# Performance work log

Measured on AMD Instinct MI355X. Metric: run time of the kernel, lower is better.

Reference implementation:

```python
import jax, jax.numpy as jnp
import numpy as np

NUM_CAPSULE = 16
DIM_CAPSULE = 32
ROUTINGS = 3
EPS = 1e-7  # K.epsilon()


def _squash(x):
    # NOTE: this repo's squash is x / sqrt(sum(x^2) + eps), i.e. pure normalization
    s = jnp.sum(jnp.square(x), axis=-1, keepdims=True)
    return x / jnp.sqrt(s + EPS)


def setup_inputs() -> dict:
    key = jax.random.key(0)
    k1, k2 = jax.random.split(key)
    B, S, D_in = 256, 512, 256
    u_vecs = jax.random.normal(k1, (B, S, D_in), dtype=jnp.float32)
    # shared conv1d kernel, kernel width 1: (1, input_dim, num_capsule*dim_capsule)
    W = jax.random.normal(k2, (1, D_in, NUM_CAPSULE * DIM_CAPSULE), dtype=jnp.float32) * 0.05
    return {"u_vecs": u_vecs, "W": W}


def reference(u_vecs, W):
    B, S, _ = u_vecs.shape
    # K.conv1d with kernel size 1 == pointwise projection
    u_hat = jnp.einsum('bsi,io->bso', u_vecs, W[0])
    # (B, S, nc*dc) -> (B, nc, S, dc)
    u_hat = u_hat.reshape(B, S, NUM_CAPSULE, DIM_CAPSULE).transpose(0, 2, 1, 3)
    b = jnp.zeros((B, NUM_CAPSULE, S), dtype=u_hat.dtype)
    outputs = None
    for i in range(ROUTINGS):
        # softmax over the num_capsule axis (permute->softmax(last)->permute back)
        c = jax.nn.softmax(b, axis=1)  # (B, nc, S)
        outputs = _squash(jnp.einsum('bni,bnid->bnd', c, u_hat))  # (B, nc, dc)
        if i < ROUTINGS - 1:
            b = jnp.einsum('bnd,bnid->bni', outputs, u_hat)
    return outputs
```

## Files before the change

kernel.cpp:

```cpp
#include <hip/hip_runtime.h>


#define SDIM 512
#define DIN  256
#define NCAP 16
#define DCAP 32
#define OC   512

typedef __attribute__((ext_vector_type(8))) __bf16 bf16x8;
typedef __attribute__((ext_vector_type(4))) float f32x4;
typedef __attribute__((ext_vector_type(4))) unsigned short u16x4;

static_assert(sizeof(bf16x8) == 16, "bf16x8 must be 16B");

__device__ __forceinline__ unsigned short f2bf(float f) {
  unsigned u = __float_as_uint(f);
  u += 0x7FFFu + ((u >> 16) & 1u);
  return (unsigned short)(u >> 16);
}

__global__ __launch_bounds__(1024) void caps_fused(
    const float* __restrict__ Uall, const float* __restrict__ Wg,
    float* __restrict__ outp)
{
  __shared__ __align__(16) unsigned short sU16[64 * 256];
  __shared__ __align__(16) unsigned short sWt16[16 * 256];
  __shared__ __align__(16) unsigned short sCT16[16 * 64];
  __shared__ __align__(16) float sV[16 * 256];
  __shared__ __align__(16) float sOut[512];

  float* sSS = (float*)sCT16;

  const int tid = threadIdx.x;
  const int w = tid >> 6;
  const int l = tid & 63;
  const int b = blockIdx.x;
  const float* U = Uall + (size_t)b * (SDIM * DIN);
  const float4* g4 = (const float4*)U;

  {
    float4 a = make_float4(0.f, 0.f, 0.f, 0.f);
    const int base = (w * 32) * 64 + l;
    #pragma unroll 8
    for (int r = 0; r < 32; ++r) {
      float4 v = g4[base + r * 64];
      a.x += v.x; a.y += v.y; a.z += v.z; a.w += v.w;
    }
    *(float4*)&sV[w * 256 + 4 * l] = a;
  }
  __syncthreads();
  if (tid < 256) {
    float s = 0.f;
    #pragma unroll
    for (int q = 0; q < 16; ++q) s += sV[q * 256 + tid];
    sSS[tid] = s * (1.0f / 16.0f);
  }
  __syncthreads();

  auto outCompute = [&](int mode) {
    if (tid < 512) {
      const int c = tid;
      const int n = c >> 5;
      float p0 = 0.f, p1 = 0.f, p2 = 0.f, p3 = 0.f;
      #pragma unroll 4
      for (int i = 0; i < 256; i += 4) {
        float x0 = mode ? sV[n * 256 + i + 0] : sSS[i + 0];
        float x1 = mode ? sV[n * 256 + i + 1] : sSS[i + 1];
        float x2 = mode ? sV[n * 256 + i + 2] : sSS[i + 2];
        float x3 = mode ? sV[n * 256 + i + 3] : sSS[i + 3];
        p0 = fmaf(Wg[(i + 0) * OC + c], x0, p0);
        p1 = fmaf(Wg[(i + 1) * OC + c], x1, p1);
        p2 = fmaf(Wg[(i + 2) * OC + c], x2, p2);
        p3 = fmaf(Wg[(i + 3) * OC + c], x3, p3);
      }
      float p = (p0 + p1) + (p2 + p3);
      float sq = p * p;
      #pragma unroll
      for (int off = 1; off < 32; off <<= 1) sq += __shfl_xor(sq, off);
      sOut[c] = p * rsqrtf(sq + 1e-7f);
    }
    __syncthreads();
  };

  auto wtCompute = [&]() {
    const int f4 = tid & 127;
    const int rr = tid >> 7;
    const float4 ov = *(const float4*)&sOut[4 * f4];
    #pragma unroll 4
    for (int it = 0; it < 32; ++it) {
      const int i = it * 8 + rr;
      const float4 wv = *(const float4*)&Wg[i * OC + 4 * f4];
      float p = wv.x * ov.x + wv.y * ov.y + wv.z * ov.z + wv.w * ov.w;
      p += __shfl_xor(p, 1);
      p += __shfl_xor(p, 2);
      p += __shfl_xor(p, 4);
      if ((f4 & 7) == 0) {
        const int n = f4 >> 3;
        sWt16[(n * 256 + i) ^ ((n & 7) << 3)] = f2bf(p);
      }
    }
    __syncthreads();
  };

  auto stage = [&](const float4* pre) {
    #pragma unroll
    for (int k = 0; k < 4; ++k) {
      const int s = w + 16 * k;
      u16x4 h;
      h[0] = f2bf(pre[k].x); h[1] = f2bf(pre[k].y);
      h[2] = f2bf(pre[k].z); h[3] = f2bf(pre[k].w);
      *(u16x4*)&sU16[(s * 256 + 4 * l) ^ ((s & 7) << 3)] = h;
    }
  };

  auto pass = [&]() {
    f32x4 vacc = {0.f, 0.f, 0.f, 0.f};
    const int nr = l & 15;
    const int grp = l >> 4;
    {
      float4 pre[4];
      #pragma unroll
      for (int k = 0; k < 4; ++k) pre[k] = g4[(w + 16 * k) * 64 + l];
      stage(pre);
    }
    __syncthreads();
    for (int chunk = 0; chunk < 8; ++chunk) {
      float4 nxt[4];
      if (chunk < 7) {
        #pragma unroll
        for (int k = 0; k < 4; ++k)
          nxt[k] = g4[((chunk + 1) * 64 + w + 16 * k) * 64 + l];
      }
      if (w < 4) {
        f32x4 y = {0.f, 0.f, 0.f, 0.f};
        const int arow = 16 * w + nr;
        #pragma unroll
        for (int ks = 0; ks < 8; ++ks) {
          bf16x8 a = *(const bf16x8*)&sU16[(arow * 256 + ks * 32 + grp * 8) ^ ((arow & 7) << 3)];
          bf16x8 bw = *(const bf16x8*)&sWt16[(nr * 256 + ks * 32 + grp * 8) ^ ((nr & 7) << 3)];
          y = __builtin_amdgcn_mfma_f32_16x16x32_bf16(a, bw, y, 0, 0, 0);
        }
        float y0 = y[0], y1 = y[1], y2 = y[2], y3 = y[3];
        float m0 = y0, m1 = y1, m2 = y2, m3 = y3;
        #pragma unroll
        for (int off = 1; off < 16; off <<= 1) {
          m0 = fmaxf(m0, __shfl_xor(m0, off));
          m1 = fmaxf(m1, __shfl_xor(m1, off));
          m2 = fmaxf(m2, __shfl_xor(m2, off));
          m3 = fmaxf(m3, __shfl_xor(m3, off));
        }
        float e0 = __expf(y0 - m0), e1 = __expf(y1 - m1);
        float e2 = __expf(y2 - m2), e3 = __expf(y3 - m3);
        float s0 = e0, s1 = e1, s2 = e2, s3 = e3;
        #pragma unroll
        for (int off = 1; off < 16; off <<= 1) {
          s0 += __shfl_xor(s0, off);
          s1 += __shfl_xor(s1, off);
          s2 += __shfl_xor(s2, off);
          s3 += __shfl_xor(s3, off);
        }
        u16x4 cw;
        cw[0] = f2bf(e0 / s0); cw[1] = f2bf(e1 / s1);
        cw[2] = f2bf(e2 / s2); cw[3] = f2bf(e3 / s3);
        *(u16x4*)&sCT16[(nr * 64 + 16 * w + 4 * grp) ^ ((nr & 7) << 3)] = cw;
      }
      __syncthreads();
      {
        const int icol = 16 * w + nr;
        #pragma unroll
        for (int ks = 0; ks < 2; ++ks) {
          bf16x8 a = *(const bf16x8*)&sCT16[(nr * 64 + ks * 32 + grp * 8) ^ ((nr & 7) << 3)];
          bf16x8 bb;
          const int s0b = ks * 32 + grp * 8;
          #pragma unroll
          for (int j = 0; j < 8; ++j) {
            unsigned short v = sU16[((s0b + j) * 256 + icol) ^ (j << 3)];
            bb[j] = __builtin_bit_cast(__bf16, v);
          }
          vacc = __builtin_amdgcn_mfma_f32_16x16x32_bf16(a, bb, vacc, 0, 0, 0);
        }
      }
      __syncthreads();
      if (chunk < 7) stage(nxt);
      __syncthreads();
    }
    #pragma unroll
    for (int r = 0; r < 4; ++r) sV[(grp * 4 + r) * 256 + 16 * w + nr] = vacc[r];
    __syncthreads();
  };

  outCompute(0);
  wtCompute();
  pass();
  outCompute(1);
  wtCompute();
  pass();
  outCompute(1);

  if (tid < 512) outp[(size_t)b * 512 + tid] = sOut[tid];
}

extern "C" void kernel_launch(void* const* d_in, const int* in_sizes, int n_in,
                              void* d_out, int out_size, void* d_ws, size_t ws_size,
                              hipStream_t stream) {
  const float* u = (const float*)d_in[0];
  const float* Wg = (const float*)d_in[1];
  float* out = (float*)d_out;
  dim3 grid(256), block(1024);
  hipLaunchKernelGGL(caps_fused, grid, block, 0, stream, u, Wg, out);
}
```

Baseline: 262.1 us.

## Warp-specialize U staging with double-buffered 128-row LDS chunks

Waves are split into roles: waves 8-15 load and convert the next 128-row chunk of U into a second LDS buffer while waves 0-7 run the logit MFMAs and softmax on the current chunk. Chunks grow from 64 to 128 rows and syncs per chunk drop from three to two, which cuts barrier count and overlaps global loads with compute. The first chunk is prefetched into registers before the out/Wt setup, and the second pass's first chunk is staged during the tail of the first pass. The change needs about 160KB of dynamic LDS and drops the max-subtraction from the softmax, which risks overflow if logits grow large.

```diff
diff --git a/kernel.cpp b/kernel.cpp
--- a/kernel.cpp
+++ b/kernel.cpp
@@ -1,11 +1,11 @@
 #include <hip/hip_runtime.h>
 
 
-#define SDIM 512
-#define DIN  256
-#define NCAP 16
-#define DCAP 32
-#define OC   512
+#define SROWS 512
+#define DIN   256
+#define OC    512
+#define CH    128
+#define NCH   4
 
 typedef __attribute__((ext_vector_type(8))) __bf16 bf16x8;
 typedef __attribute__((ext_vector_type(4))) float f32x4;
@@ -19,27 +19,27 @@
   return (unsigned short)(u >> 16);
 }
 
-__global__ __launch_bounds__(1024) void caps_fused(
+
+__global__ __launch_bounds__(1024) void caps_main(
     const float* __restrict__ Uall, const float* __restrict__ Wg,
     float* __restrict__ outp)
 {
-  __shared__ __align__(16) unsigned short sU16[64 * 256];
-  __shared__ __align__(16) unsigned short sWt16[16 * 256];
-  __shared__ __align__(16) unsigned short sCT16[16 * 64];
-  __shared__ __align__(16) float sV[16 * 256];
-  __shared__ __align__(16) float sOut[512];
-
-  float* sSS = (float*)sCT16;
+  extern __shared__ char smem[];
+  unsigned short* sU  = (unsigned short*)smem;
+  unsigned short* sWt = (unsigned short*)(smem + 131072);
+  unsigned short* sCT = (unsigned short*)(smem + 139264);
+  float* sV   = (float*)(smem + 143360);
+  float* sOut = (float*)(smem + 159744);
+  float* sSS  = (float*)(smem + 139264);
 
   const int tid = threadIdx.x;
-  const int w = tid >> 6;
-  const int l = tid & 63;
+  const int w = tid >> 6, l = tid & 63;
+  const int nr = l & 15, g = l >> 4;
   const int b = blockIdx.x;
-  const float* U = Uall + (size_t)b * (SDIM * DIN);
-  const float4* g4 = (const float4*)U;
+  const float4* g4 = (const float4*)(Uall + (size_t)b * (SROWS * DIN));
 
   {
-    float4 a = make_float4(0.f, 0.f, 0.f, 0.f);
+    float4 a = {0.f, 0.f, 0.f, 0.f};
     const int base = (w * 32) * 64 + l;
     #pragma unroll 8
     for (int r = 0; r < 32; ++r) {
@@ -57,10 +57,13 @@
   }
   __syncthreads();
 
+  float4 pre[8];
+  #pragma unroll
+  for (int k = 0; k < 8; ++k) pre[k] = g4[(w * 8 + k) * 64 + l];
+
   auto outCompute = [&](int mode) {
     if (tid < 512) {
-      const int c = tid;
-      const int n = c >> 5;
+      const int c = tid, n = c >> 5;
       float p0 = 0.f, p1 = 0.f, p2 = 0.f, p3 = 0.f;
       #pragma unroll 4
       for (int i = 0; i < 256; i += 4) {
@@ -96,105 +99,101 @@
       p += __shfl_xor(p, 4);
       if ((f4 & 7) == 0) {
         const int n = f4 >> 3;
-        sWt16[(n * 256 + i) ^ ((n & 7) << 3)] = f2bf(p);
+        sWt[(n * 256 + i) ^ ((n & 7) << 3)] = f2bf(p);
       }
     }
     __syncthreads();
   };
 
-  auto stage = [&](const float4* pre) {
-    #pragma unroll
-    for (int k = 0; k < 4; ++k) {
-      const int s = w + 16 * k;
+  auto writePre = [&]() {
+    #pragma unroll
+    for (int k = 0; k < 8; ++k) {
+      const int rl = w * 8 + k;
       u16x4 h;
       h[0] = f2bf(pre[k].x); h[1] = f2bf(pre[k].y);
       h[2] = f2bf(pre[k].z); h[3] = f2bf(pre[k].w);
-      *(u16x4*)&sU16[(s * 256 + 4 * l) ^ ((s & 7) << 3)] = h;
-    }
-  };
-
-  auto pass = [&]() {
+      *(u16x4*)&sU[(rl * 256 + 4 * l) ^ ((rl & 7) << 3)] = h;
+    }
+  };
+
+  auto stage8 = [&](int p, int rbase) {
+    const int wi = w - 8;
+    #pragma unroll
+    for (int h = 0; h < 2; ++h) {
+      float4 v[8];
+      #pragma unroll
+      for (int k = 0; k < 8; ++k) v[k] = g4[(rbase + wi * 16 + h * 8 + k) * 64 + l];
+      #pragma unroll
+      for (int k = 0; k < 8; ++k) {
+        const int rl = wi * 16 + h * 8 + k;
+        u16x4 hh;
+        hh[0] = f2bf(v[k].x); hh[1] = f2bf(v[k].y);
+        hh[2] = f2bf(v[k].z); hh[3] = f2bf(v[k].w);
+        *(u16x4*)&sU[p * 32768 + ((rl * 256 + 4 * l) ^ ((rl & 7) << 3))] = hh;
+      }
+    }
+  };
+
+  auto pass = [&](bool stageNext) {
     f32x4 vacc = {0.f, 0.f, 0.f, 0.f};
-    const int nr = l & 15;
-    const int grp = l >> 4;
-    {
-      float4 pre[4];
-      #pragma unroll
-      for (int k = 0; k < 4; ++k) pre[k] = g4[(w + 16 * k) * 64 + l];
-      stage(pre);
-    }
-    __syncthreads();
-    for (int chunk = 0; chunk < 8; ++chunk) {
-      float4 nxt[4];
-      if (chunk < 7) {
-        #pragma unroll
-        for (int k = 0; k < 4; ++k)
-          nxt[k] = g4[((chunk + 1) * 64 + w + 16 * k) * 64 + l];
-      }
-      if (w < 4) {
+    for (int c = 0; c < NCH; ++c) {
+      const int p = c & 1;
+      if (w >= 8) {
+        if (c < NCH - 1)      stage8(p ^ 1, (c + 1) * CH);
+        else if (stageNext)   stage8(p ^ 1, 0);
+      } else {
         f32x4 y = {0.f, 0.f, 0.f, 0.f};
         const int arow = 16 * w + nr;
+        const int asw = (nr & 7) << 3;
         #pragma unroll
         for (int ks = 0; ks < 8; ++ks) {
-          bf16x8 a = *(const bf16x8*)&sU16[(arow * 256 + ks * 32 + grp * 8) ^ ((arow & 7) << 3)];
-          bf16x8 bw = *(const bf16x8*)&sWt16[(nr * 256 + ks * 32 + grp * 8) ^ ((nr & 7) << 3)];
+          bf16x8 a  = *(const bf16x8*)&sU[p * 32768 + ((arow * 256 + ks * 32 + g * 8) ^ asw)];
+          bf16x8 bw = *(const bf16x8*)&sWt[(nr * 256 + ks * 32 + g * 8) ^ asw];
           y = __builtin_amdgcn_mfma_f32_16x16x32_bf16(a, bw, y, 0, 0, 0);
         }
-        float y0 = y[0], y1 = y[1], y2 = y[2], y3 = y[3];
-        float m0 = y0, m1 = y1, m2 = y2, m3 = y3;
-        #pragma unroll
-        for (int off = 1; off < 16; off <<= 1) {
-          m0 = fmaxf(m0, __shfl_xor(m0, off));
-          m1 = fmaxf(m1, __shfl_xor(m1, off));
-          m2 = fmaxf(m2, __shfl_xor(m2, off));
-          m3 = fmaxf(m3, __shfl_xor(m3, off));
-        }
-        float e0 = __expf(y0 - m0), e1 = __expf(y1 - m1);
-        float e2 = __expf(y2 - m2), e3 = __expf(y3 - m3);
+        float e0 = __expf(y[0]), e1 = __expf(y[1]), e2 = __expf(y[2]), e3 = __expf(y[3]);
         float s0 = e0, s1 = e1, s2 = e2, s3 = e3;
         #pragma unroll
         for (int off = 1; off < 16; off <<= 1) {
-          s0 += __shfl_xor(s0, off);
-          s1 += __shfl_xor(s1, off);
-          s2 += __shfl_xor(s2, off);
-          s3 += __shfl_xor(s3, off);
+          s0 += __shfl_xor(s0, off); s1 += __shfl_xor(s1, off);
+          s2 += __shfl_xor(s2, off); s3 += __shfl_xor(s3, off);
         }
         u16x4 cw;
         cw[0] = f2bf(e0 / s0); cw[1] = f2bf(e1 / s1);
         cw[2] = f2bf(e2 / s2); cw[3] = f2bf(e3 / s3);
-        *(u16x4*)&sCT16[(nr * 64 + 16 * w + 4 * grp) ^ ((nr & 7) << 3)] = cw;
+        *(u16x4*)&sCT[(nr * 128 + 16 * w + 4 * g) ^ asw] = cw;
       }
       __syncthreads();
       {
         const int icol = 16 * w + nr;
         #pragma unroll
-        for (int ks = 0; ks < 2; ++ks) {
-          bf16x8 a = *(const bf16x8*)&sCT16[(nr * 64 + ks * 32 + grp * 8) ^ ((nr & 7) << 3)];
+        for (int ks = 0; ks < 4; ++ks) {
+          bf16x8 a = *(const bf16x8*)&sCT[(nr * 128 + ks * 32 + g * 8) ^ ((nr & 7) << 3)];
           bf16x8 bb;
-          const int s0b = ks * 32 + grp * 8;
           #pragma unroll
           for (int j = 0; j < 8; ++j) {
-            unsigned short v = sU16[((s0b + j) * 256 + icol) ^ (j << 3)];
-            bb[j] = __builtin_bit_cast(__bf16, v);
+            const int s = ks * 32 + g * 8 + j;
+            bb[j] = __builtin_bit_cast(__bf16,
+                     sU[p * 32768 + ((s * 256 + icol) ^ ((s & 7) << 3))]);
           }
           vacc = __builtin_amdgcn_mfma_f32_16x16x32_bf16(a, bb, vacc, 0, 0, 0);
         }
       }
       __syncthreads();
-      if (chunk < 7) stage(nxt);
-      __syncthreads();
-    }
-    #pragma unroll
-    for (int r = 0; r < 4; ++r) sV[(grp * 4 + r) * 256 + 16 * w + nr] = vacc[r];
+    }
+    #pragma unroll
+    for (int r = 0; r < 4; ++r) sV[(4 * g + r) * 256 + 16 * w + nr] = vacc[r];
     __syncthreads();
   };
 
   outCompute(0);
   wtCompute();
-  pass();
+  writePre();
+  __syncthreads();
+  pass(true);
   outCompute(1);
   wtCompute();
-  pass();
+  pass(false);
   outCompute(1);
 
   if (tid < 512) outp[(size_t)b * 512 + tid] = sOut[tid];
@@ -203,9 +202,11 @@
 extern "C" void kernel_launch(void* const* d_in, const int* in_sizes, int n_in,
                               void* d_out, int out_size, void* d_ws, size_t ws_size,
                               hipStream_t stream) {
-  const float* u = (const float*)d_in[0];
+  const float* u  = (const float*)d_in[0];
   const float* Wg = (const float*)d_in[1];
   float* out = (float*)d_out;
-  dim3 grid(256), block(1024);
-  hipLaunchKernelGGL(caps_fused, grid, block, 0, stream, u, Wg, out);
+  (void)d_ws; (void)ws_size;
+  hipFuncSetAttribute(reinterpret_cast<const void*>(caps_main),
+                      hipFuncAttributeMaxDynamicSharedMemorySize, 161792);
+  caps_main<<<dim3(256), dim3(1024), 161792, stream>>>(u, Wg, out);
 }
```

Measured after the change: 279.3 us. +6.6%, slower.

## Split fused capsule routing into multi-kernel pipeline with row-split parallelism

Applied to the files above, without the earlier changes.

Replaces the single per-batch fused kernel (256 blocks of 1024 threads) with a sequence of kernels: a column-sum kernel, a routing kernel that computes squashed outputs and W·out projections, and a pass kernel that splits each batch's 512 sequence rows across 4 blocks and writes partial sums to workspace. This is meant to raise the number of concurrently active blocks and cut per-block serialization, at the cost of extra launches and global round-trips through workspace. It also drops the max-subtraction in the softmax, relying on logits being bounded because the outputs are normalized. The old fused kernel is kept as a fallback when the workspace is too small.

```diff
diff --git a/kernel.cpp b/kernel.cpp
--- a/kernel.cpp
+++ b/kernel.cpp
@@ -1,22 +1,205 @@
 #include <hip/hip_runtime.h>
 
 
-#define SDIM 512
-#define DIN  256
-#define NCAP 16
-#define DCAP 32
-#define OC   512
+#define DIN   256
+#define OC    512
+#define SROWS 512
 
 typedef __attribute__((ext_vector_type(8))) __bf16 bf16x8;
 typedef __attribute__((ext_vector_type(4))) float f32x4;
 typedef __attribute__((ext_vector_type(4))) unsigned short u16x4;
-
-static_assert(sizeof(bf16x8) == 16, "bf16x8 must be 16B");
 
 __device__ __forceinline__ unsigned short f2bf(float f) {
   unsigned u = __float_as_uint(f);
   u += 0x7FFFu + ((u >> 16) & 1u);
   return (unsigned short)(u >> 16);
+}
+
+#define SWZ(r) ((((r) ^ ((r) >> 3)) & 7) << 3)
+
+__global__ __launch_bounds__(256) void k_colsum(
+    const float* __restrict__ Uall, float* __restrict__ cpart)
+{
+  __shared__ float sA[4][256];
+  const int t = blockIdx.x, b = blockIdx.y;
+  const int tid = threadIdx.x;
+  const int c4 = tid & 63, rq = tid >> 6;
+  const float4* g4 = (const float4*)(Uall + (size_t)b * (SROWS * DIN));
+  const int R0 = t * 128;
+  float4 a = {0.f, 0.f, 0.f, 0.f};
+  #pragma unroll 8
+  for (int k = 0; k < 32; ++k) {
+    float4 v = g4[(R0 + rq + 4 * k) * 64 + c4];
+    a.x += v.x; a.y += v.y; a.z += v.z; a.w += v.w;
+  }
+  *(float4*)&sA[rq][4 * c4] = a;
+  __syncthreads();
+  if (tid < 64) {
+    float4 s = {0.f, 0.f, 0.f, 0.f};
+    #pragma unroll
+    for (int q = 0; q < 4; ++q) {
+      float4 v = *(float4*)&sA[q][4 * tid];
+      s.x += v.x; s.y += v.y; s.z += v.z; s.w += v.w;
+    }
+    *(float4*)&cpart[(size_t)(b * 4 + t) * 256 + 4 * tid] = s;
+  }
+}
+
+__global__ __launch_bounds__(512) void k_route(
+    const float* __restrict__ W, const float* __restrict__ src,
+    unsigned short* __restrict__ wt, float* __restrict__ outF,
+    int mode, int final_)
+{
+  __shared__ float sV[16 * 256];
+  __shared__ float sP[2][512];
+  __shared__ float sOut[512];
+  const int b = blockIdx.x;
+  const int tid = threadIdx.x;
+
+  if (mode == 0) {
+    if (tid < 256) {
+      float v = 0.f;
+      #pragma unroll
+      for (int t = 0; t < 4; ++t) v += src[(size_t)(b * 4 + t) * 256 + tid];
+      #pragma unroll
+      for (int n = 0; n < 16; ++n) sV[n * 256 + tid] = v;
+    }
+  } else {
+    #pragma unroll
+    for (int qq = 0; qq < 2; ++qq) {
+      const int q = 2 * tid + qq;
+      f32x4 s = {0.f, 0.f, 0.f, 0.f};
+      #pragma unroll
+      for (int t = 0; t < 4; ++t)
+        s += *(const f32x4*)&src[(size_t)(b * 4 + t) * 4096 + 4 * q];
+      *(f32x4*)&sV[4 * q] = s;
+    }
+  }
+  __syncthreads();
+
+  {
+    const int pair = tid & 255, half = tid >> 8;
+    const int c0 = pair * 2, n = c0 >> 5;
+    float p0 = 0.f, p1 = 0.f;
+    const int i0 = half * 128;
+    #pragma unroll 8
+    for (int i = i0; i < i0 + 128; ++i) {
+      const float2 wv = *(const float2*)&W[(size_t)i * OC + c0];
+      const float x = sV[n * 256 + i];
+      p0 = fmaf(wv.x, x, p0);
+      p1 = fmaf(wv.y, x, p1);
+    }
+    sP[half][c0] = p0; sP[half][c0 + 1] = p1;
+  }
+  __syncthreads();
+
+  {
+    const float p = sP[0][tid] + sP[1][tid];
+    float sq = p * p;
+    #pragma unroll
+    for (int off = 1; off < 32; off <<= 1) sq += __shfl_xor(sq, off);
+    const float o = p * rsqrtf(sq + 1e-7f);
+    if (final_) { outF[(size_t)b * 512 + tid] = o; return; }
+    sOut[tid] = o;
+  }
+  __syncthreads();
+
+  {
+    const int f4i = tid & 127, rr = tid >> 7;
+    const int n = f4i >> 3;
+    const float4 ov = *(const float4*)&sOut[4 * f4i];
+    #pragma unroll 4
+    for (int it = 0; it < 64; ++it) {
+      const int i = it * 4 + rr;
+      const float4 wv = *(const float4*)&W[(size_t)i * OC + 4 * f4i];
+      float p = wv.x * ov.x + wv.y * ov.y + wv.z * ov.z + wv.w * ov.w;
+      p += __shfl_xor(p, 1);
+      p += __shfl_xor(p, 2);
+      p += __shfl_xor(p, 4);
+      if ((tid & 7) == 0)
+        wt[(size_t)b * 4096 + n * 256 + i] = f2bf(p);
+    }
+  }
+}
+
+__global__ __launch_bounds__(512, 4) void k_pass(
+    const float* __restrict__ Uall, const unsigned short* __restrict__ wt,
+    float* __restrict__ vpart)
+{
+  extern __shared__ char smem[];
+  unsigned short* sU  = (unsigned short*)smem;
+  unsigned short* sWt = (unsigned short*)(smem + 65536);
+  unsigned short* sCT = (unsigned short*)(smem + 73728);
+
+  const int t = blockIdx.x, b = blockIdx.y;
+  const int tid = threadIdx.x;
+  const int w = tid >> 6, l = tid & 63;
+  const int nr = l & 15, g = l >> 4;
+  const float4* g4 = (const float4*)(Uall + (size_t)b * (SROWS * DIN));
+  const int R0 = t * 128;
+
+  {
+    const int n = tid >> 5, i0 = (tid & 31) * 8;
+    const uint4 wv = *(const uint4*)&wt[(size_t)b * 4096 + n * 256 + i0];
+    *(uint4*)&sWt[(n * 256 + i0) ^ SWZ(n)] = wv;
+  }
+  #pragma unroll 4
+  for (int k = 0; k < 16; ++k) {
+    const int row = w * 16 + k;
+    const float4 v = g4[(R0 + row) * 64 + l];
+    u16x4 h;
+    h[0] = f2bf(v.x); h[1] = f2bf(v.y); h[2] = f2bf(v.z); h[3] = f2bf(v.w);
+    *(u16x4*)&sU[(row * 256 + 4 * l) ^ SWZ(row)] = h;
+  }
+  __syncthreads();
+
+  {
+    f32x4 y = {0.f, 0.f, 0.f, 0.f};
+    const int arow = 16 * w + nr;
+    #pragma unroll
+    for (int ks = 0; ks < 8; ++ks) {
+      bf16x8 a  = *(const bf16x8*)&sU[(arow * 256 + ks * 32 + g * 8) ^ SWZ(arow)];
+      bf16x8 bw = *(const bf16x8*)&sWt[(nr * 256 + ks * 32 + g * 8) ^ SWZ(nr)];
+      y = __builtin_amdgcn_mfma_f32_16x16x32_bf16(a, bw, y, 0, 0, 0);
+    }
+    float e0 = __expf(y[0]), e1 = __expf(y[1]), e2 = __expf(y[2]), e3 = __expf(y[3]);
+    float s0 = e0, s1 = e1, s2 = e2, s3 = e3;
+    #pragma unroll
+    for (int off = 1; off < 16; off <<= 1) {
+      s0 += __shfl_xor(s0, off); s1 += __shfl_xor(s1, off);
+      s2 += __shfl_xor(s2, off); s3 += __shfl_xor(s3, off);
+    }
+    u16x4 cw;
+    cw[0] = f2bf(e0 / s0); cw[1] = f2bf(e1 / s1);
+    cw[2] = f2bf(e2 / s2); cw[3] = f2bf(e3 / s3);
+    *(u16x4*)&sCT[(nr * 128 + 16 * w + 4 * g) ^ SWZ(nr)] = cw;
+  }
+  __syncthreads();
+
+  {
+    const int icol0 = 32 * w + nr, icol1 = icol0 + 16;
+    f32x4 v0 = {0.f, 0.f, 0.f, 0.f}, v1 = {0.f, 0.f, 0.f, 0.f};
+    #pragma unroll
+    for (int ks = 0; ks < 4; ++ks) {
+      bf16x8 a = *(const bf16x8*)&sCT[(nr * 128 + ks * 32 + g * 8) ^ SWZ(nr)];
+      bf16x8 b0, b1;
+      #pragma unroll
+      for (int j = 0; j < 8; ++j) {
+        const int s = ks * 32 + g * 8 + j;
+        b0[j] = __builtin_bit_cast(__bf16, sU[(s * 256 + icol0) ^ SWZ(s)]);
+        b1[j] = __builtin_bit_cast(__bf16, sU[(s * 256 + icol1) ^ SWZ(s)]);
+      }
+      v0 = __builtin_amdgcn_mfma_f32_16x16x32_bf16(a, b0, v0, 0, 0, 0);
+      v1 = __builtin_amdgcn_mfma_f32_16x16x32_bf16(a, b1, v1, 0, 0, 0);
+    }
+    float* vp = vpart + (size_t)(b * 4 + t) * 4096;
+    #pragma unroll
+    for (int r = 0; r < 4; ++r) {
+      const int n = 4 * g + r;
+      vp[n * 256 + icol0] = v0[r];
+      vp[n * 256 + icol1] = v1[r];
+    }
+  }
 }
 
 __global__ __launch_bounds__(1024) void caps_fused(
@@ -28,14 +211,12 @@
   __shared__ __align__(16) unsigned short sCT16[16 * 64];
   __shared__ __align__(16) float sV[16 * 256];
   __shared__ __align__(16) float sOut[512];
-
   float* sSS = (float*)sCT16;
 
   const int tid = threadIdx.x;
-  const int w = tid >> 6;
-  const int l = tid & 63;
+  const int w = tid >> 6, l = tid & 63;
   const int b = blockIdx.x;
-  const float* U = Uall + (size_t)b * (SDIM * DIN);
+  const float* U = Uall + (size_t)b * (SROWS * DIN);
   const float4* g4 = (const float4*)U;
 
   {
@@ -59,8 +240,7 @@
 
   auto outCompute = [&](int mode) {
     if (tid < 512) {
-      const int c = tid;
-      const int n = c >> 5;
+      const int c = tid, n = c >> 5;
       float p0 = 0.f, p1 = 0.f, p2 = 0.f, p3 = 0.f;
       #pragma unroll 4
       for (int i = 0; i < 256; i += 4) {
@@ -140,24 +320,12 @@
           bf16x8 bw = *(const bf16x8*)&sWt16[(nr * 256 + ks * 32 + grp * 8) ^ ((nr & 7) << 3)];
           y = __builtin_amdgcn_mfma_f32_16x16x32_bf16(a, bw, y, 0, 0, 0);
         }
-        float y0 = y[0], y1 = y[1], y2 = y[2], y3 = y[3];
-        float m0 = y0, m1 = y1, m2 = y2, m3 = y3;
-        #pragma unroll
-        for (int off = 1; off < 16; off <<= 1) {
-          m0 = fmaxf(m0, __shfl_xor(m0, off));
-          m1 = fmaxf(m1, __shfl_xor(m1, off));
-          m2 = fmaxf(m2, __shfl_xor(m2, off));
-          m3 = fmaxf(m3, __shfl_xor(m3, off));
-        }
-        float e0 = __expf(y0 - m0), e1 = __expf(y1 - m1);
-        float e2 = __expf(y2 - m2), e3 = __expf(y3 - m3);
+        float e0 = __expf(y[0]), e1 = __expf(y[1]), e2 = __expf(y[2]), e3 = __expf(y[3]);
         float s0 = e0, s1 = e1, s2 = e2, s3 = e3;
         #pragma unroll
         for (int off = 1; off < 16; off <<= 1) {
-          s0 += __shfl_xor(s0, off);
-          s1 += __shfl_xor(s1, off);
-          s2 += __shfl_xor(s2, off);
-          s3 += __shfl_xor(s3, off);
+          s0 += __shfl_xor(s0, off); s1 += __shfl_xor(s1, off);
+          s2 += __shfl_xor(s2, off); s3 += __shfl_xor(s3, off);
         }
         u16x4 cw;
         cw[0] = f2bf(e0 / s0); cw[1] = f2bf(e1 / s1);
@@ -203,9 +371,30 @@
 extern "C" void kernel_launch(void* const* d_in, const int* in_sizes, int n_in,
                               void* d_out, int out_size, void* d_ws, size_t ws_size,
                               hipStream_t stream) {
-  const float* u = (const float*)d_in[0];
-  const float* Wg = (const float*)d_in[1];
+  const float* U = (const float*)d_in[0];
+  const float* W = (const float*)d_in[1];
   float* out = (float*)d_out;
-  dim3 grid(256), block(1024);
-  hipLaunchKernelGGL(caps_fused, grid, block, 0, stream, u, Wg, out);
-}
+
+  const size_t WT_OFF = 0;
+  const size_t CP_OFF = 2u * 1024 * 1024;
+  const size_t VP_OFF = 3u * 1024 * 1024;
+  const size_t NEED   = VP_OFF + 16u * 1024 * 1024;
+
+  if (ws_size < NEED) {
+    caps_fused<<<dim3(256), dim3(1024), 0, stream>>>(U, W, out);
+    return;
+  }
+  unsigned short* wt = (unsigned short*)((char*)d_ws + WT_OFF);
+  float* cpart = (float*)((char*)d_ws + CP_OFF);
+  float* vpart = (float*)((char*)d_ws + VP_OFF);
+
+  hipFuncSetAttribute(reinterpret_cast<const void*>(k_pass),
+                      hipFuncAttributeMaxDynamicSharedMemorySize, 77824);
+
+  k_colsum<<<dim3(4, 256), 256, 0, stream>>>(U, cpart);
+  k_route<<<256, 512, 0, stream>>>(W, cpart, wt, out, 0, 0);
+  k_pass<<<dim3(4, 256), 512, 77824, stream>>>(U, wt, vpart);
+  k_route<<<256, 512, 0, stream>>>(W, vpart, wt, out, 1, 0);
+  k_pass<<<dim3(4, 256), 512, 77824, stream>>>(U, wt, vpart);
+  k_route<<<256, 512, 0, stream>>>(W, vpart, wt, out, 1, 1);
+}
```

After: 315.6 us. 20.4% more time.
